# Kernel tuning notes

Measured on AMD Instinct MI355X. Metric: run time of the kernel, lower is better.

## Reference

```python
import jax, jax.numpy as jnp
import numpy as np

N_SIGMA = 1
NUM_CLASS = 1
N_INST = 16          # max instance id (ids 1..16); instances==0 is background
W_INST, W_VAR, W_SEED = 1.0, 10.0, 1.0
H, W, B = 512, 512, 8
GRID = 1024          # buffer is linspace over 1024 then cropped to H,W


def make_xym(h, w, dtype=jnp.float32):
    full = jnp.linspace(0.0, 1.0, GRID, dtype=dtype)
    xm = jnp.broadcast_to(full[:w][None, :], (h, w))   # x varies along width
    ym = jnp.broadcast_to(full[:h][:, None], (h, w))   # y varies along height
    return jnp.stack([xm, ym], axis=0)                 # [2, H, W]


def lovasz_hinge_flat(logits, labels):
    # logits: [N] float, labels: [N] float in {0,1}
    signs = 2.0 * labels - 1.0
    errors = 1.0 - logits * signs
    order = jnp.argsort(-errors)
    errors_sorted = errors[order]
    gt_sorted = labels[order]
    gts = jnp.sum(gt_sorted)
    intersection = gts - jnp.cumsum(gt_sorted)
    union = gts + jnp.cumsum(1.0 - gt_sorted)
    jaccard = 1.0 - intersection / union
    grad = jnp.concatenate([jaccard[:1], jaccard[1:] - jaccard[:-1]])
    return jnp.sum(jax.nn.relu(errors_sorted) * grad)


def _per_image(pred, instance, label, xym):
    h, w = pred.shape[1], pred.shape[2]
    spatial_emb = jnp.tanh(pred[0:2]) + xym              # [2,H,W]
    sigma = pred[2:2 + N_SIGMA]                          # [n_sigma,H,W]
    seed = jax.nn.sigmoid(pred[2 + N_SIGMA])             # [H,W] (num_class==1)

    label_mask = (label == 1)
    bg_mask = (label == 0)
    seed_loss = jnp.sum(jnp.where(bg_mask, seed ** 2, 0.0))

    ids = jnp.arange(1, N_INST + 1)
    masks = (instance[None] == ids[:, None, None]) & label_mask[None]  # [K,H,W] bool
    maskf = masks.astype(pred.dtype)
    counts = jnp.sum(maskf, axis=(1, 2))                 # [K]
    present = counts > 0
    safe = jnp.maximum(counts, 1.0)

    # to_center=True: center = mean of xym coords over each instance mask
    center = jnp.einsum('khw,chw->kc', maskf, xym) / safe[:, None]        # [K,2]
    s_mean = jnp.einsum('khw,shw->ks', maskf, sigma) / safe[:, None]      # [K,n_sigma]

    # var loss: mean over in-mask pixels of (sigma - detached mean)^2
    dev2 = (sigma[None] - jax.lax.stop_gradient(s_mean)[:, :, None, None]) ** 2  # [K,ns,H,W]
    var_terms = jnp.einsum('khw,kshw->k', maskf, dev2) / (safe * N_SIGMA)

    # dist = exp(-s * sum_c (emb_c - center_c)^2), s = exp(10 * mean sigma)
    s_exp = jnp.exp(10.0 * s_mean)[:, 0]                 # [K] (n_sigma==1 broadcasts)
    diff2 = jnp.sum((spatial_emb[None] - center[:, :, None, None]) ** 2, axis=1)  # [K,H,W]
    dist = jnp.exp(-s_exp[:, None, None] * diff2)        # [K,H,W]

    inst_losses = jax.vmap(
        lambda d, m: lovasz_hinge_flat(2.0 * d.ravel() - 1.0, m.ravel())
    )(dist, maskf)
    instance_loss = jnp.sum(jnp.where(present, inst_losses, 0.0))
    var_loss = jnp.sum(jnp.where(present, var_terms, 0.0))

    seed_loss = seed_loss + jnp.sum(
        maskf * (seed[None] - jax.lax.stop_gradient(dist)) ** 2)

    obj = jnp.maximum(jnp.sum(present.astype(pred.dtype)), 1.0)
    return (W_INST * instance_loss / obj
            + W_VAR * var_loss / obj
            + W_SEED * seed_loss / (h * w))


def setup_inputs() -> dict:
    key = jax.random.key(0)
    k1, k2, k3 = jax.random.split(key, 3)
    prediction = jax.random.normal(k1, (B, 2 + N_SIGMA + NUM_CLASS, H, W), dtype=jnp.float32)
    instances = jax.random.randint(k2, (B, H, W), 0, N_INST + 1).astype(jnp.int64)
    labels = jax.random.randint(k3, (B, H, W), 0, NUM_CLASS + 1).astype(jnp.int64)
    return {"prediction": prediction, "instances": instances, "labels": labels}


def reference(prediction, instances, labels):
    xym = make_xym(prediction.shape[2], prediction.shape[3], prediction.dtype)
    per_img = jax.vmap(_per_image, in_axes=(0, 0, 0, None))(
        prediction, instances, labels, xym)
    return jnp.mean(per_img)
```

## Files before the change

### kernel.cpp

```cpp
#include <hip/hip_runtime.h>
#include <hip/hip_fp16.h>
#include <math.h>

#define HWPX 262144
#define NIMG 8
#define ACC_STRIDE 96
#define NB 1024
#define ZMAX 8.0f
#define NSPLIT 32
#define NGRP 2
#define PREP_GRID 2048

typedef unsigned long long u64;

__device__ __forceinline__ float tanh_fast(float x) {
  float t = __expf(2.0f * x);
  return 1.0f - __fdividef(2.0f, t + 1.0f);
}
__device__ __forceinline__ float sigmoid_fast(float x) {
  return __fdividef(1.0f, 1.0f + __expf(-x));
}

template<bool PACK>
__global__ __launch_bounds__(256, 2) void k_prep(const float* __restrict__ pred,
    const int* __restrict__ inst, const int* __restrict__ lab,
    u64* __restrict__ rec, float* __restrict__ part)
{
  __shared__ float s[8][83];
  int t = threadIdx.x;
  for (int i = t; i < 8*83; i += 256) (&s[0][0])[i] = 0.0f;
  __syncthreads();
  int bid = blockIdx.x;
  int b = bid >> 8;
  int px0 = ((bid & 255) << 10) + t*4;
  const float* pb = pred + (size_t)b*4*HWPX;
  size_t ib = (size_t)b*HWPX;
  int r = t & 7;
  int w0 = px0 & 511;
  float ym = (float)(px0 >> 9) * (1.0f/1023.0f);

  float4 X  = *(const float4*)(pb + px0);
  float4 Y  = *(const float4*)(pb + HWPX + px0);
  float4 Gv = *(const float4*)(pb + 2*HWPX + px0);
  float4 Q  = *(const float4*)(pb + 3*HWPX + px0);
  int4   L  = *(const int4*)(lab + ib + px0);
  int4   I  = *(const int4*)(inst + ib + px0);

  float bg = 0.0f;
  u64 rv0 = 0, rv1 = 0, rv2 = 0, rv3 = 0;

#define PXB(RV, C, XX, YY, GG, QQ, LL, II) { \
    float xm = (float)(w0 + C) * (1.0f/1023.0f); \
    float sd = sigmoid_fast(QQ); \
    int mid = ((LL) == 1 && (unsigned)((II)-1) < 16u) ? (II) : 0; \
    if (PACK) { \
      float ex = tanh_fast(XX) + xm; \
      float ey = tanh_fast(YY) + ym; \
      RV = (u64)__half_as_ushort(__float2half(ex)) \
         | ((u64)__half_as_ushort(__float2half(ey)) << 16) \
         | ((u64)__half_as_ushort(__float2half(sd)) << 32) \
         | ((u64)mid << 48); \
    } \
    if ((LL) == 0) { bg += sd*sd; } \
    else if (mid) { int k = mid - 1; \
      atomicAdd(&s[r][k], 1.0f); \
      atomicAdd(&s[r][16+k], xm); \
      atomicAdd(&s[r][32+k], ym); \
      atomicAdd(&s[r][48+k], GG); \
      atomicAdd(&s[r][64+k], (GG)*(GG)); } }

  PXB(rv0, 0, X.x, Y.x, Gv.x, Q.x, L.x, I.x)
  PXB(rv1, 1, X.y, Y.y, Gv.y, Q.y, L.y, I.y)
  PXB(rv2, 2, X.z, Y.z, Gv.z, Q.z, L.z, I.z)
  PXB(rv3, 3, X.w, Y.w, Gv.w, Q.w, L.w, I.w)
#undef PXB

  if (PACK) {
    ulonglong2* rp = (ulonglong2*)(rec + ib + px0);
    rp[0] = make_ulonglong2(rv0, rv1);
    rp[1] = make_ulonglong2(rv2, rv3);
  }
  #pragma unroll
  for (int o = 32; o > 0; o >>= 1) bg += __shfl_down(bg, o);
  if ((t & 63) == 0) atomicAdd(&s[0][80], bg);
  __syncthreads();
  if (t < 96) {
    float v = 0.0f;
    if (t < 83) {
      #pragma unroll
      for (int rr = 0; rr < 8; ++rr) v += s[rr][t];
    }
    part[(size_t)bid*96 + t] = v;
  }
}

__global__ __launch_bounds__(1024) void k_fin(const float* __restrict__ part,
    double* __restrict__ accd, float* __restrict__ pairinfo)
{
  __shared__ float red2[10*96];
  int t = threadIdx.x, b = blockIdx.x;
  if (t < 960) {
    int e = t % 96, c = t / 96;
    int lo = c*26, hi = lo + 26; if (hi > 256) hi = 256;
    const float* pp = part + (size_t)b*256*96 + e;
    float v = 0.0f;
    for (int blk = lo; blk < hi; ++blk) v += pp[(size_t)blk*96];
    red2[c*96 + e] = v;
  }
  __syncthreads();
  if (t < 96) {
    float v = 0.0f;
    #pragma unroll
    for (int cc = 0; cc < 10; ++cc) v += red2[cc*96 + t];
    red2[t] = v;
  }
  __syncthreads();
  if (t < 16) {
    float cnt = red2[t];
    float safe = cnt > 0.0f ? cnt : 1.0f;
    float sm = red2[48+t] / safe;
    float4 pi = make_float4(red2[16+t]/safe, red2[32+t]/safe, __expf(10.0f*sm), cnt);
    ((float4*)pairinfo)[b*16 + t] = pi;
  }
  if (t == 0) {
    double vs = 0.0; float np = 0.0f;
    for (int k2 = 0; k2 < 16; ++k2) {
      float cnt = red2[k2];
      if (cnt > 0.0f) {
        np += 1.0f;
        float ssg = red2[48+k2];
        float var = (red2[64+k2] - ssg*ssg/cnt) / cnt;
        if (var < 0.0f) var = 0.0f;
        vs += (double)var;
      }
    }
    double* ab = accd + (size_t)b*ACC_STRIDE;
    ab[80] = (double)red2[80];
    ab[81] = 0.0;
    ab[82] = 0.0;
    ab[83] = vs;
    ab[84] = np > 1.0f ? (double)np : 1.0;
  }
}

__global__ __launch_bounds__(1024) void k_hist(const u64* __restrict__ rec,
    const float* __restrict__ pairinfo,
    unsigned* __restrict__ partial, double* __restrict__ accd)
{
  __shared__ unsigned hist[8*NB];
  __shared__ float redf[16];
  int t = threadIdx.x, bid = blockIdx.x;
  int b = bid & 7;
  int rr = bid >> 3;
  int g = rr & 1;
  int s = rr >> 1;
  for (int i = t; i < 8*NB; i += 1024) hist[i] = 0u;
  float cx[8], cy[8], se[8], s128[8];
  #pragma unroll
  for (int j = 0; j < 8; ++j) {
    float4 pi = ((const float4*)pairinfo)[b*16 + g*8 + j];
    cx[j] = pi.x; cy[j] = pi.y; se[j] = pi.z; s128[j] = pi.z * (float)(NB/ZMAX);
  }
  __syncthreads();
  size_t base = (size_t)b*HWPX + (size_t)s*(HWPX/NSPLIT);
  float fit = 0.0f;
  for (int it = 0; it < HWPX/NSPLIT/2048; ++it) {
    size_t px = base + it*2048 + t*2;
    ulonglong2 v2 = *((const ulonglong2*)(rec + px));
    u64 vv[2] = {v2.x, v2.y};
    #pragma unroll
    for (int c = 0; c < 2; ++c) {
      u64 v = vv[c];
      float ex = __half2float(__ushort_as_half((unsigned short)(v & 0xffffu)));
      float ey = __half2float(__ushort_as_half((unsigned short)((v >> 16) & 0xffffu)));
      float sd = __half2float(__ushort_as_half((unsigned short)((v >> 32) & 0xffffu)));
      int rel = (int)(v >> 48) - 1 - g*8;
      #pragma unroll
      for (int j = 0; j < 8; ++j) {
        float dx = ex - cx[j], dy = ey - cy[j];
        float d2 = fmaf(dx, dx, dy*dy);
        int key; unsigned add;
        if (rel == j) {
          float d = __expf(-d2 * se[j]);
          float e = fmaf(-2.0f, d, 2.0f);
          int kk = (int)(e * (float)(NB/2));
          key = kk > NB-1 ? NB-1 : kk;
          add = 0x10000u;
          float df = sd - d; fit += df*df;
        } else {
          key = (int)fminf(d2 * s128[j], (float)(NB-1));
          add = 1u;
        }
        atomicAdd(&hist[j*NB + key], add);
      }
    }
  }
  #pragma unroll
  for (int o = 32; o > 0; o >>= 1) fit += __shfl_down(fit, o);
  if ((t & 63) == 0) redf[t >> 6] = fit;
  __syncthreads();
  if (t == 0) {
    float ft = 0.0f;
    for (int i = 0; i < 16; ++i) ft += redf[i];
    atomicAdd(&accd[(size_t)b*ACC_STRIDE + 81], (double)ft);
  }
  unsigned* pp = partial + (size_t)((b*NGRP + g)*NSPLIT + s)*(8*NB);
  for (int i = t; i < 8*NB; i += 1024) pp[i] = hist[i];
}

__global__ __launch_bounds__(1024) void k_scan(const unsigned* __restrict__ partial,
    const float* __restrict__ pairinfo, double* __restrict__ accd)
{
  __shared__ unsigned sp[NB], sq[NB];
  __shared__ float red[16];
  int t = threadIdx.x, bid = blockIdx.x;
  int b = bid >> 4, k = bid & 15;
  int g = k >> 3, j8 = k & 7;
  float G = pairinfo[(b*16 + k)*4 + 3];
  if (G <= 0.0f) return;
  sq[t] = 0u;
  __syncthreads();
  unsigned p = 0, q = 0;
  const unsigned* basep = partial + (size_t)((b*NGRP + g)*NSPLIT)*(8*NB) + j8*NB + t;
  #pragma unroll 4
  for (int s2 = 0; s2 < NSPLIT; ++s2) {
    unsigned h = basep[(size_t)s2*(8*NB)];
    p += h >> 16; q += h & 0xffffu;
  }
  float zmid = (t + 0.5f) * (ZMAX/NB);
  float ev = 2.0f * __expf(-zmid);
  int eb = (int)(ev * (float)(NB/2));
  if (eb > NB-1) eb = NB-1;
  if (q) atomicAdd(&sq[eb], q);
  __syncthreads();
  unsigned qe = sq[t];
  __syncthreads();
  int j = (NB-1) - t;
  sp[j] = p; sq[j] = qe;
  __syncthreads();
  for (int off = 1; off < NB; off <<= 1) {
    unsigned vp = 0, vq = 0;
    if (j >= off) { vp = sp[j-off]; vq = sq[j-off]; }
    __syncthreads();
    sp[j] += vp; sq[j] += vq;
    __syncthreads();
  }
  float A  = (float)(sp[j] - p);
  float Bn = (float)(sq[j] - qe);
  float val = (t + 0.5f) * (2.0f/NB);
  float pf = (float)p, qf = (float)qe;
  float Jb = (A + Bn) / (G + Bn);
  float Ja = (A + Bn + pf + qf) / (G + Bn + qf);
  float contrib = val * (Ja - Jb);
  #pragma unroll
  for (int o = 32; o > 0; o >>= 1) contrib += __shfl_down(contrib, o);
  if ((t & 63) == 0) red[t >> 6] = contrib;
  __syncthreads();
  if (t == 0) {
    float tot = 0.0f;
    for (int i = 0; i < 16; ++i) tot += red[i];
    atomicAdd(&accd[(size_t)b*ACC_STRIDE + 82], (double)tot);
  }
}

__global__ __launch_bounds__(1024) void k_lov_old(const float* __restrict__ pred,
    const int* __restrict__ inst, const int* __restrict__ lab,
    const float* __restrict__ pairinfo, double* __restrict__ accd)
{
  constexpr int SHIFT = 18;
  constexpr int NBB = (0x40000000 >> SHIFT) + 1;
  extern __shared__ unsigned char smem[];
  unsigned* histP = reinterpret_cast<unsigned*>(smem);
  unsigned* histQ = histP + NBB;
  unsigned* scanP = histQ + NBB;
  unsigned* scanQ = scanP + 1024;
  float* red  = reinterpret_cast<float*>(scanQ + 1024);
  float* redf = red + 16;
  int t = threadIdx.x, bid = blockIdx.x;
  int b = bid >> 4, k = bid & 15;
  float4 pi = reinterpret_cast<const float4*>(pairinfo)[bid];
  float cx = pi.x, cy = pi.y, sexp = pi.z, G = pi.w;
  if (G <= 0.0f) return;
  for (int i = t; i < 2*NBB; i += 1024) histP[i] = 0u;
  __syncthreads();
  size_t ib = (size_t)b * HWPX;
  const float* pb = pred + (size_t)b * 4 * HWPX;
  const int target = k + 1;
  float fit = 0.0f;
  for (int j = 0; j < HWPX/1024; ++j) {
    int px = (j << 10) + t;
    int h = px >> 9, w = px & 511;
    float ex = tanhf(pb[px]) + w*(1.0f/1023.0f);
    float ey = tanhf(pb[HWPX+px]) + h*(1.0f/1023.0f);
    float sd = 1.0f/(1.0f + __expf(-pb[3*HWPX+px]));
    int lv = lab[ib+px], iv = inst[ib+px];
    float dx = ex - cx, dy = ey - cy;
    float d = __expf(-sexp * (dx*dx + dy*dy));
    bool m = (lv == 1) && (iv == target);
    float e = m ? fmaf(-2.0f, d, 2.0f) : 2.0f * d;
    unsigned key = __float_as_uint(e) >> SHIFT;
    atomicAdd(m ? &histP[key] : &histQ[key], 1u);
    if (m) { float df = sd - d; fit += df*df; }
  }
  #pragma unroll
  for (int o = 32; o > 0; o >>= 1) fit += __shfl_down(fit, o);
  if ((t & 63) == 0) redf[t >> 6] = fit;
  __syncthreads();
  constexpr int CB = NBB / 1024;
  int start = (NBB - 1) - t * CB;
  int nk = (t == 1023) ? (CB + 1) : CB;
  unsigned lp = 0, lq = 0;
  for (int i = 0; i < nk; ++i) { lp += histP[start-i]; lq += histQ[start-i]; }
  scanP[t] = lp; scanQ[t] = lq;
  __syncthreads();
  for (int off = 1; off < 1024; off <<= 1) {
    unsigned vp = 0, vq = 0;
    if (t >= off) { vp = scanP[t-off]; vq = scanQ[t-off]; }
    __syncthreads();
    scanP[t] += vp; scanQ[t] += vq;
    __syncthreads();
  }
  float A  = (float)(scanP[t] - lp);
  float Bn = (float)(scanQ[t] - lq);
  float contrib = 0.0f;
  for (int i = 0; i < nk; ++i) {
    int kk = start - i;
    unsigned p = histP[kk], q = histQ[kk];
    if (p | q) {
      float lo = __uint_as_float((unsigned)kk << SHIFT);
      float hi = __uint_as_float((unsigned)(kk+1) << SHIFT);
      float valv = 0.5f*(lo+hi);
      if (valv > 2.0f) valv = 2.0f;
      float pq = (float)(p + q), qf = (float)q;
      float Jb = (A + Bn) / (G + Bn);
      float Ja = (A + Bn + pq) / (G + Bn + qf);
      contrib += valv * (Ja - Jb);
      A += (float)p; Bn += qf;
    }
  }
  #pragma unroll
  for (int o = 32; o > 0; o >>= 1) contrib += __shfl_down(contrib, o);
  if ((t & 63) == 0) red[t >> 6] = contrib;
  __syncthreads();
  if (t == 0) {
    float tot = 0.0f, ft = 0.0f;
    for (int i = 0; i < 16; ++i) { tot += red[i]; ft += redf[i]; }
    atomicAdd(&accd[(size_t)b*ACC_STRIDE + 82], (double)tot);
    atomicAdd(&accd[(size_t)b*ACC_STRIDE + 81], (double)ft);
  }
}

__global__ void k_final(const double* __restrict__ accd, float* __restrict__ out)
{
  int t = threadIdx.x;
  double lb = 0.0;
  if (t < NIMG) {
    const double* ab = accd + (size_t)t*ACC_STRIDE;
    lb = (ab[82] + 10.0*ab[83]) / ab[84] + (ab[80] + ab[81]) * (1.0/(double)HWPX);
  }
  #pragma unroll
  for (int o = 4; o > 0; o >>= 1) lb += __shfl_down(lb, o);
  if (t == 0) out[0] = (float)(lb * 0.125);
}

extern "C" void kernel_launch(void* const* d_in, const int* in_sizes, int n_in,
                              void* d_out, int out_size, void* d_ws, size_t ws_size,
                              hipStream_t stream)
{
  const float* pred = (const float*)d_in[0];
  const int*   inst = (const int*)d_in[1];
  const int*   lab  = (const int*)d_in[2];
  float* out = (float*)d_out;

  size_t recB   = (size_t)NIMG * HWPX * sizeof(u64);
  size_t partB  = (size_t)NIMG * NGRP * NSPLIT * 8 * NB * 4;
  size_t pstatB = (size_t)PREP_GRID * 96 * sizeof(float);
  size_t accB   = (size_t)NIMG * ACC_STRIDE * sizeof(double);
  size_t pairB  = 128 * 4 * sizeof(float);
  bool full = ws_size >= recB + partB + pstatB + accB + pairB;

  char* ws = (char*)d_ws;
  if (full) {
    u64*      rec   = (u64*)ws;
    unsigned* part  = (unsigned*)(ws + recB);
    float*    pstat = (float*)(ws + recB + partB);
    double*   accd  = (double*)(ws + recB + partB + pstatB);
    float*    pairinfo = (float*)(ws + recB + partB + pstatB + accB);
    k_prep<true><<<PREP_GRID,256,0,stream>>>(pred, inst, lab, rec, pstat);
    k_fin<<<NIMG,1024,0,stream>>>(pstat, accd, pairinfo);
    k_hist<<<NIMG*NGRP*NSPLIT,1024,0,stream>>>(rec, pairinfo, part, accd);
    k_scan<<<128,1024,0,stream>>>(part, pairinfo, accd);
    k_final<<<1,64,0,stream>>>(accd, out);
  } else {
    float*    pstat = (float*)ws;
    double*   accd  = (double*)(ws + pstatB);
    float*    pairinfo = (float*)(ws + pstatB + accB);
    k_prep<false><<<PREP_GRID,256,0,stream>>>(pred, inst, lab, nullptr, pstat);
    k_fin<<<NIMG,1024,0,stream>>>(pstat, accd, pairinfo);
    size_t lds18 = ((size_t)2*4097 + 2048)*4 + 128;
    k_lov_old<<<128,1024,lds18,stream>>>(pred, inst, lab, pairinfo, accd);
    k_final<<<1,64,0,stream>>>(accd, out);
  }
}
```

Baseline: 73.55 us.

## Recompute embeddings in histogram kernel instead of storing packed fp16 records

Drops the intermediate packed fp16 record buffer. The histogram kernel now reads the raw prediction, instance and label arrays and recomputes tanh, sigmoid and embeddings itself, covering all 16 instances per block rather than splitting them into two groups of 8. Histogram resolution is halved to 512 bins and the split count doubled, so each block handles 4 pixels per thread, and the scan kernel runs with 512 threads. This removes the 16MB record write and read, at the cost of more transcendental math per pixel-instance pair and coarser loss quantisation.

```diff
diff --git a/kernel.cpp b/kernel.cpp
--- a/kernel.cpp
+++ b/kernel.cpp
@@ -1,14 +1,12 @@
 #include <hip/hip_runtime.h>
-#include <hip/hip_fp16.h>
 #include <math.h>
 
 #define HWPX 262144
 #define NIMG 8
 #define ACC_STRIDE 96
-#define NB 1024
+#define NB 512
 #define ZMAX 8.0f
-#define NSPLIT 32
-#define NGRP 2
+#define NSPLIT 64
 #define PREP_GRID 2048
 
 typedef unsigned long long u64;
@@ -21,10 +19,9 @@
   return __fdividef(1.0f, 1.0f + __expf(-x));
 }
 
-template<bool PACK>
-__global__ __launch_bounds__(256, 2) void k_prep(const float* __restrict__ pred,
+__global__ __launch_bounds__(256) void k_stats(const float* __restrict__ pred,
     const int* __restrict__ inst, const int* __restrict__ lab,
-    u64* __restrict__ rec, float* __restrict__ part)
+    float* __restrict__ part)
 {
   __shared__ float s[8][83];
   int t = threadIdx.x;
@@ -39,47 +36,28 @@
   int w0 = px0 & 511;
   float ym = (float)(px0 >> 9) * (1.0f/1023.0f);
 
-  float4 X  = *(const float4*)(pb + px0);
-  float4 Y  = *(const float4*)(pb + HWPX + px0);
   float4 Gv = *(const float4*)(pb + 2*HWPX + px0);
   float4 Q  = *(const float4*)(pb + 3*HWPX + px0);
   int4   L  = *(const int4*)(lab + ib + px0);
   int4   I  = *(const int4*)(inst + ib + px0);
 
   float bg = 0.0f;
-  u64 rv0 = 0, rv1 = 0, rv2 = 0, rv3 = 0;
-
-#define PXB(RV, C, XX, YY, GG, QQ, LL, II) { \
+#define PXS(C, GG, QQ, LL, II) { \
     float xm = (float)(w0 + C) * (1.0f/1023.0f); \
-    float sd = sigmoid_fast(QQ); \
     int mid = ((LL) == 1 && (unsigned)((II)-1) < 16u) ? (II) : 0; \
-    if (PACK) { \
-      float ex = tanh_fast(XX) + xm; \
-      float ey = tanh_fast(YY) + ym; \
-      RV = (u64)__half_as_ushort(__float2half(ex)) \
-         | ((u64)__half_as_ushort(__float2half(ey)) << 16) \
-         | ((u64)__half_as_ushort(__float2half(sd)) << 32) \
-         | ((u64)mid << 48); \
-    } \
-    if ((LL) == 0) { bg += sd*sd; } \
+    if ((LL) == 0) { float sd = sigmoid_fast(QQ); bg += sd*sd; } \
     else if (mid) { int k = mid - 1; \
       atomicAdd(&s[r][k], 1.0f); \
       atomicAdd(&s[r][16+k], xm); \
       atomicAdd(&s[r][32+k], ym); \
       atomicAdd(&s[r][48+k], GG); \
       atomicAdd(&s[r][64+k], (GG)*(GG)); } }
-
-  PXB(rv0, 0, X.x, Y.x, Gv.x, Q.x, L.x, I.x)
-  PXB(rv1, 1, X.y, Y.y, Gv.y, Q.y, L.y, I.y)
-  PXB(rv2, 2, X.z, Y.z, Gv.z, Q.z, L.z, I.z)
-  PXB(rv3, 3, X.w, Y.w, Gv.w, Q.w, L.w, I.w)
-#undef PXB
-
-  if (PACK) {
-    ulonglong2* rp = (ulonglong2*)(rec + ib + px0);
-    rp[0] = make_ulonglong2(rv0, rv1);
-    rp[1] = make_ulonglong2(rv2, rv3);
-  }
+  PXS(0, Gv.x, Q.x, L.x, I.x)
+  PXS(1, Gv.y, Q.y, L.y, I.y)
+  PXS(2, Gv.z, Q.z, L.z, I.z)
+  PXS(3, Gv.w, Q.w, L.w, I.w)
+#undef PXS
+
   #pragma unroll
   for (int o = 32; o > 0; o >>= 1) bg += __shfl_down(bg, o);
   if ((t & 63) == 0) atomicAdd(&s[0][80], bg);
@@ -143,58 +121,60 @@
   }
 }
 
-__global__ __launch_bounds__(1024) void k_hist(const u64* __restrict__ rec,
+__global__ __launch_bounds__(1024, 4) void k_hist(const float* __restrict__ pred,
+    const int* __restrict__ inst, const int* __restrict__ lab,
     const float* __restrict__ pairinfo,
     unsigned* __restrict__ partial, double* __restrict__ accd)
 {
-  __shared__ unsigned hist[8*NB];
+  __shared__ unsigned hist[16*NB];
   __shared__ float redf[16];
   int t = threadIdx.x, bid = blockIdx.x;
   int b = bid & 7;
-  int rr = bid >> 3;
-  int g = rr & 1;
-  int s = rr >> 1;
-  for (int i = t; i < 8*NB; i += 1024) hist[i] = 0u;
-  float cx[8], cy[8], se[8], s128[8];
-  #pragma unroll
-  for (int j = 0; j < 8; ++j) {
-    float4 pi = ((const float4*)pairinfo)[b*16 + g*8 + j];
-    cx[j] = pi.x; cy[j] = pi.y; se[j] = pi.z; s128[j] = pi.z * (float)(NB/ZMAX);
-  }
-  __syncthreads();
-  size_t base = (size_t)b*HWPX + (size_t)s*(HWPX/NSPLIT);
+  int s = bid >> 3;
+  for (int i = t; i < 16*NB; i += 1024) hist[i] = 0u;
+  float cx[16], cy[16], s128[16];
+  #pragma unroll
+  for (int j = 0; j < 16; ++j) {
+    float4 pi = ((const float4*)pairinfo)[b*16 + j];
+    cx[j] = pi.x; cy[j] = pi.y; s128[j] = pi.z * (float)(NB/ZMAX);
+  }
+  __syncthreads();
+  int px0 = s*(HWPX/NSPLIT) + t*4;
+  const float* pb = pred + (size_t)b*4*HWPX;
+  size_t ib = (size_t)b*HWPX;
+  float4 X = *(const float4*)(pb + px0);
+  float4 Y = *(const float4*)(pb + HWPX + px0);
+  float4 Q = *(const float4*)(pb + 3*HWPX + px0);
+  int4   L = *(const int4*)(lab + ib + px0);
+  int4   I = *(const int4*)(inst + ib + px0);
+  int w0 = px0 & 511;
+  float ym = (float)(px0 >> 9) * (1.0f/1023.0f);
   float fit = 0.0f;
-  for (int it = 0; it < HWPX/NSPLIT/2048; ++it) {
-    size_t px = base + it*2048 + t*2;
-    ulonglong2 v2 = *((const ulonglong2*)(rec + px));
-    u64 vv[2] = {v2.x, v2.y};
-    #pragma unroll
-    for (int c = 0; c < 2; ++c) {
-      u64 v = vv[c];
-      float ex = __half2float(__ushort_as_half((unsigned short)(v & 0xffffu)));
-      float ey = __half2float(__ushort_as_half((unsigned short)((v >> 16) & 0xffffu)));
-      float sd = __half2float(__ushort_as_half((unsigned short)((v >> 32) & 0xffffu)));
-      int rel = (int)(v >> 48) - 1 - g*8;
-      #pragma unroll
-      for (int j = 0; j < 8; ++j) {
-        float dx = ex - cx[j], dy = ey - cy[j];
-        float d2 = fmaf(dx, dx, dy*dy);
-        int key; unsigned add;
-        if (rel == j) {
-          float d = __expf(-d2 * se[j]);
-          float e = fmaf(-2.0f, d, 2.0f);
-          int kk = (int)(e * (float)(NB/2));
-          key = kk > NB-1 ? NB-1 : kk;
-          add = 0x10000u;
-          float df = sd - d; fit += df*df;
-        } else {
-          key = (int)fminf(d2 * s128[j], (float)(NB-1));
-          add = 1u;
-        }
-        atomicAdd(&hist[j*NB + key], add);
-      }
-    }
-  }
+
+#define PXH(C, XX, YY, QQ, LL, II) { \
+    float xm = (float)(w0 + C) * (1.0f/1023.0f); \
+    float exf = tanh_fast(XX) + xm; \
+    float eyf = tanh_fast(YY) + ym; \
+    float sd = sigmoid_fast(QQ); \
+    int rel = ((LL) == 1 && (unsigned)((II)-1) < 16u) ? ((II)-1) : -1; \
+    _Pragma("unroll") \
+    for (int j = 0; j < 16; ++j) { \
+      float dx = exf - cx[j], dy = eyf - cy[j]; \
+      float z = fmaf(dx, dx, dy*dy) * s128[j]; \
+      float d = __expf(-z * (ZMAX/(float)NB)); \
+      bool m = (j == rel); \
+      float e = fmaf(-2.0f, d, 2.0f); \
+      int kp = (int)(e * (float)(NB/2)); kp = kp > NB-1 ? NB-1 : kp; \
+      int kn = (int)fminf(z, (float)(NB-1)); \
+      atomicAdd(&hist[j*NB + (m ? kp : kn)], m ? 0x10000u : 1u); \
+      if (m) { float df = sd - d; fit += df*df; } \
+    } }
+  PXH(0, X.x, Y.x, Q.x, L.x, I.x)
+  PXH(1, X.y, Y.y, Q.y, L.y, I.y)
+  PXH(2, X.z, Y.z, Q.z, L.z, I.z)
+  PXH(3, X.w, Y.w, Q.w, L.w, I.w)
+#undef PXH
+
   #pragma unroll
   for (int o = 32; o > 0; o >>= 1) fit += __shfl_down(fit, o);
   if ((t & 63) == 0) redf[t >> 6] = fit;
@@ -204,27 +184,26 @@
     for (int i = 0; i < 16; ++i) ft += redf[i];
     atomicAdd(&accd[(size_t)b*ACC_STRIDE + 81], (double)ft);
   }
-  unsigned* pp = partial + (size_t)((b*NGRP + g)*NSPLIT + s)*(8*NB);
-  for (int i = t; i < 8*NB; i += 1024) pp[i] = hist[i];
-}
-
-__global__ __launch_bounds__(1024) void k_scan(const unsigned* __restrict__ partial,
+  unsigned* pp = partial + (size_t)(b*NSPLIT + s)*(16*NB);
+  for (int i = t; i < 16*NB; i += 1024) pp[i] = hist[i];
+}
+
+__global__ __launch_bounds__(512) void k_scan(const unsigned* __restrict__ partial,
     const float* __restrict__ pairinfo, double* __restrict__ accd)
 {
   __shared__ unsigned sp[NB], sq[NB];
-  __shared__ float red[16];
+  __shared__ float red[8];
   int t = threadIdx.x, bid = blockIdx.x;
   int b = bid >> 4, k = bid & 15;
-  int g = k >> 3, j8 = k & 7;
   float G = pairinfo[(b*16 + k)*4 + 3];
   if (G <= 0.0f) return;
   sq[t] = 0u;
   __syncthreads();
   unsigned p = 0, q = 0;
-  const unsigned* basep = partial + (size_t)((b*NGRP + g)*NSPLIT)*(8*NB) + j8*NB + t;
+  const unsigned* basep = partial + (size_t)(b*NSPLIT)*(16*NB) + k*NB + t;
   #pragma unroll 4
   for (int s2 = 0; s2 < NSPLIT; ++s2) {
-    unsigned h = basep[(size_t)s2*(8*NB)];
+    unsigned h = basep[(size_t)s2*(16*NB)];
     p += h >> 16; q += h & 0xffffu;
   }
   float zmid = (t + 0.5f) * (ZMAX/NB);
@@ -258,7 +237,7 @@
   __syncthreads();
   if (t == 0) {
     float tot = 0.0f;
-    for (int i = 0; i < 16; ++i) tot += red[i];
+    for (int i = 0; i < 8; ++i) tot += red[i];
     atomicAdd(&accd[(size_t)b*ACC_STRIDE + 82], (double)tot);
   }
 }
@@ -372,30 +351,28 @@
   const int*   lab  = (const int*)d_in[2];
   float* out = (float*)d_out;
 
-  size_t recB   = (size_t)NIMG * HWPX * sizeof(u64);
-  size_t partB  = (size_t)NIMG * NGRP * NSPLIT * 8 * NB * 4;
+  size_t partB  = (size_t)NIMG * NSPLIT * 16 * NB * 4;
   size_t pstatB = (size_t)PREP_GRID * 96 * sizeof(float);
   size_t accB   = (size_t)NIMG * ACC_STRIDE * sizeof(double);
   size_t pairB  = 128 * 4 * sizeof(float);
-  bool full = ws_size >= recB + partB + pstatB + accB + pairB;
+  bool full = ws_size >= partB + pstatB + accB + pairB;
 
   char* ws = (char*)d_ws;
   if (full) {
-    u64*      rec   = (u64*)ws;
-    unsigned* part  = (unsigned*)(ws + recB);
-    float*    pstat = (float*)(ws + recB + partB);
-    double*   accd  = (double*)(ws + recB + partB + pstatB);
-    float*    pairinfo = (float*)(ws + recB + partB + pstatB + accB);
-    k_prep<true><<<PREP_GRID,256,0,stream>>>(pred, inst, lab, rec, pstat);
+    unsigned* part  = (unsigned*)ws;
+    float*    pstat = (float*)(ws + partB);
+    double*   accd  = (double*)(ws + partB + pstatB);
+    float*    pairinfo = (float*)(ws + partB + pstatB + accB);
+    k_stats<<<PREP_GRID,256,0,stream>>>(pred, inst, lab, pstat);
     k_fin<<<NIMG,1024,0,stream>>>(pstat, accd, pairinfo);
-    k_hist<<<NIMG*NGRP*NSPLIT,1024,0,stream>>>(rec, pairinfo, part, accd);
-    k_scan<<<128,1024,0,stream>>>(part, pairinfo, accd);
+    k_hist<<<NIMG*NSPLIT,1024,0,stream>>>(pred, inst, lab, pairinfo, part, accd);
+    k_scan<<<128,512,0,stream>>>(part, pairinfo, accd);
     k_final<<<1,64,0,stream>>>(accd, out);
   } else {
     float*    pstat = (float*)ws;
     double*   accd  = (double*)(ws + pstatB);
     float*    pairinfo = (float*)(ws + pstatB + accB);
-    k_prep<false><<<PREP_GRID,256,0,stream>>>(pred, inst, lab, nullptr, pstat);
+    k_stats<<<PREP_GRID,256,0,stream>>>(pred, inst, lab, pstat);
     k_fin<<<NIMG,1024,0,stream>>>(pstat, accd, pairinfo);
     size_t lds18 = ((size_t)2*4097 + 2048)*4 + 128;
     k_lov_old<<<128,1024,lds18,stream>>>(pred, inst, lab, pairinfo, accd);
```

After: 81.75 us. +11.2%, slower.

## Re-partition prep and histogram grids to cut partial buffers and reduction work

Applied to the files above, without the earlier changes.

k_prep now runs 256 blocks of 1024 threads, each thread handling 8 pixels with scalar coalesced loads. This cuts the per-block statistics partials from 2048 to 256, so k_fin becomes a small 128-thread single-pass reduction. k_hist halves NSPLIT, which halves the number of 32KB per-block histograms written to global memory and later read by k_scan. The cost is fewer blocks, about one per CU, which gives less latency hiding. The vector float4/ulonglong2 loads are also replaced by scalar loads.

```diff
diff --git a/kernel.cpp b/kernel.cpp
--- a/kernel.cpp
+++ b/kernel.cpp
@@ -7,9 +7,9 @@
 #define ACC_STRIDE 96
 #define NB 1024
 #define ZMAX 8.0f
-#define NSPLIT 32
+#define NSPLIT 16
 #define NGRP 2
-#define PREP_GRID 2048
+#define PREP_BLOCKS 256
 
 typedef unsigned long long u64;
 
@@ -22,63 +22,52 @@
 }
 
 template<bool PACK>
-__global__ __launch_bounds__(256, 2) void k_prep(const float* __restrict__ pred,
+__global__ __launch_bounds__(1024) void k_prep(const float* __restrict__ pred,
     const int* __restrict__ inst, const int* __restrict__ lab,
     u64* __restrict__ rec, float* __restrict__ part)
 {
   __shared__ float s[8][83];
   int t = threadIdx.x;
-  for (int i = t; i < 8*83; i += 256) (&s[0][0])[i] = 0.0f;
+  for (int i = t; i < 8*83; i += 1024) (&s[0][0])[i] = 0.0f;
   __syncthreads();
   int bid = blockIdx.x;
-  int b = bid >> 8;
-  int px0 = ((bid & 255) << 10) + t*4;
+  int b = bid >> 5;
+  int chunk = bid & 31;
   const float* pb = pred + (size_t)b*4*HWPX;
   size_t ib = (size_t)b*HWPX;
   int r = t & 7;
-  int w0 = px0 & 511;
-  float ym = (float)(px0 >> 9) * (1.0f/1023.0f);
-
-  float4 X  = *(const float4*)(pb + px0);
-  float4 Y  = *(const float4*)(pb + HWPX + px0);
-  float4 Gv = *(const float4*)(pb + 2*HWPX + px0);
-  float4 Q  = *(const float4*)(pb + 3*HWPX + px0);
-  int4   L  = *(const int4*)(lab + ib + px0);
-  int4   I  = *(const int4*)(inst + ib + px0);
-
   float bg = 0.0f;
-  u64 rv0 = 0, rv1 = 0, rv2 = 0, rv3 = 0;
-
-#define PXB(RV, C, XX, YY, GG, QQ, LL, II) { \
-    float xm = (float)(w0 + C) * (1.0f/1023.0f); \
-    float sd = sigmoid_fast(QQ); \
-    int mid = ((LL) == 1 && (unsigned)((II)-1) < 16u) ? (II) : 0; \
-    if (PACK) { \
-      float ex = tanh_fast(XX) + xm; \
-      float ey = tanh_fast(YY) + ym; \
-      RV = (u64)__half_as_ushort(__float2half(ex)) \
-         | ((u64)__half_as_ushort(__float2half(ey)) << 16) \
-         | ((u64)__half_as_ushort(__float2half(sd)) << 32) \
-         | ((u64)mid << 48); \
-    } \
-    if ((LL) == 0) { bg += sd*sd; } \
-    else if (mid) { int k = mid - 1; \
-      atomicAdd(&s[r][k], 1.0f); \
-      atomicAdd(&s[r][16+k], xm); \
-      atomicAdd(&s[r][32+k], ym); \
-      atomicAdd(&s[r][48+k], GG); \
-      atomicAdd(&s[r][64+k], (GG)*(GG)); } }
-
-  PXB(rv0, 0, X.x, Y.x, Gv.x, Q.x, L.x, I.x)
-  PXB(rv1, 1, X.y, Y.y, Gv.y, Q.y, L.y, I.y)
-  PXB(rv2, 2, X.z, Y.z, Gv.z, Q.z, L.z, I.z)
-  PXB(rv3, 3, X.w, Y.w, Gv.w, Q.w, L.w, I.w)
-#undef PXB
-
-  if (PACK) {
-    ulonglong2* rp = (ulonglong2*)(rec + ib + px0);
-    rp[0] = make_ulonglong2(rv0, rv1);
-    rp[1] = make_ulonglong2(rv2, rv3);
+  #pragma unroll
+  for (int j = 0; j < 8; ++j) {
+    int px = (chunk << 13) + (j << 10) + t;
+    float X = pb[px];
+    float Y = pb[HWPX + px];
+    float Gv = pb[2*HWPX + px];
+    float Q = pb[3*HWPX + px];
+    int L = lab[ib + px];
+    int I = inst[ib + px];
+    int w = px & 511, h = px >> 9;
+    float xm = (float)w * (1.0f/1023.0f), ym = (float)h * (1.0f/1023.0f);
+    float sd = sigmoid_fast(Q);
+    int mid = (L == 1 && (unsigned)(I-1) < 16u) ? I : 0;
+    if (PACK) {
+      float ex = tanh_fast(X) + xm;
+      float ey = tanh_fast(Y) + ym;
+      rec[ib + px] = (u64)__half_as_ushort(__float2half(ex))
+                   | ((u64)__half_as_ushort(__float2half(ey)) << 16)
+                   | ((u64)__half_as_ushort(__float2half(sd)) << 32)
+                   | ((u64)mid << 48);
+    }
+    if (L == 0) {
+      bg += sd*sd;
+    } else if (mid) {
+      int k = mid - 1;
+      atomicAdd(&s[r][k], 1.0f);
+      atomicAdd(&s[r][16+k], xm);
+      atomicAdd(&s[r][32+k], ym);
+      atomicAdd(&s[r][48+k], Gv);
+      atomicAdd(&s[r][64+k], Gv*Gv);
+    }
   }
   #pragma unroll
   for (int o = 32; o > 0; o >>= 1) bg += __shfl_down(bg, o);
@@ -86,7 +75,7 @@
   __syncthreads();
   if (t < 96) {
     float v = 0.0f;
-    if (t < 83) {
+    if (t < 81) {
       #pragma unroll
       for (int rr = 0; rr < 8; ++rr) v += s[rr][t];
     }
@@ -94,48 +83,40 @@
   }
 }
 
-__global__ __launch_bounds__(1024) void k_fin(const float* __restrict__ part,
+__global__ __launch_bounds__(128) void k_fin(const float* __restrict__ part,
     double* __restrict__ accd, float* __restrict__ pairinfo)
 {
-  __shared__ float red2[10*96];
+  __shared__ float red[96];
   int t = threadIdx.x, b = blockIdx.x;
-  if (t < 960) {
-    int e = t % 96, c = t / 96;
-    int lo = c*26, hi = lo + 26; if (hi > 256) hi = 256;
-    const float* pp = part + (size_t)b*256*96 + e;
-    float v = 0.0f;
-    for (int blk = lo; blk < hi; ++blk) v += pp[(size_t)blk*96];
-    red2[c*96 + e] = v;
-  }
-  __syncthreads();
   if (t < 96) {
     float v = 0.0f;
-    #pragma unroll
-    for (int cc = 0; cc < 10; ++cc) v += red2[cc*96 + t];
-    red2[t] = v;
+    const float* pp = part + (size_t)b*32*96 + t;
+    #pragma unroll 8
+    for (int blk = 0; blk < 32; ++blk) v += pp[(size_t)blk*96];
+    red[t] = v;
   }
   __syncthreads();
   if (t < 16) {
-    float cnt = red2[t];
+    float cnt = red[t];
     float safe = cnt > 0.0f ? cnt : 1.0f;
-    float sm = red2[48+t] / safe;
-    float4 pi = make_float4(red2[16+t]/safe, red2[32+t]/safe, __expf(10.0f*sm), cnt);
+    float sm = red[48+t] / safe;
+    float4 pi = make_float4(red[16+t]/safe, red[32+t]/safe, __expf(10.0f*sm), cnt);
     ((float4*)pairinfo)[b*16 + t] = pi;
   }
   if (t == 0) {
     double vs = 0.0; float np = 0.0f;
     for (int k2 = 0; k2 < 16; ++k2) {
-      float cnt = red2[k2];
+      float cnt = red[k2];
       if (cnt > 0.0f) {
         np += 1.0f;
-        float ssg = red2[48+k2];
-        float var = (red2[64+k2] - ssg*ssg/cnt) / cnt;
+        float ssg = red[48+k2];
+        float var = (red[64+k2] - ssg*ssg/cnt) / cnt;
         if (var < 0.0f) var = 0.0f;
         vs += (double)var;
       }
     }
     double* ab = accd + (size_t)b*ACC_STRIDE;
-    ab[80] = (double)red2[80];
+    ab[80] = (double)red[80];
     ab[81] = 0.0;
     ab[82] = 0.0;
     ab[83] = vs;
@@ -159,40 +140,36 @@
   #pragma unroll
   for (int j = 0; j < 8; ++j) {
     float4 pi = ((const float4*)pairinfo)[b*16 + g*8 + j];
-    cx[j] = pi.x; cy[j] = pi.y; se[j] = pi.z; s128[j] = pi.z * (float)(NB/ZMAX);
+    cx[j] = pi.x; cy[j] = pi.y; se[j] = pi.z; s128[j] = pi.z * ((float)NB/ZMAX);
   }
   __syncthreads();
   size_t base = (size_t)b*HWPX + (size_t)s*(HWPX/NSPLIT);
   float fit = 0.0f;
-  for (int it = 0; it < HWPX/NSPLIT/2048; ++it) {
-    size_t px = base + it*2048 + t*2;
-    ulonglong2 v2 = *((const ulonglong2*)(rec + px));
-    u64 vv[2] = {v2.x, v2.y};
+  #pragma unroll 2
+  for (int it = 0; it < HWPX/NSPLIT/1024; ++it) {
+    size_t px = base + it*1024 + t;
+    u64 v = rec[px];
+    float ex = __half2float(__ushort_as_half((unsigned short)(v & 0xffffu)));
+    float ey = __half2float(__ushort_as_half((unsigned short)((v >> 16) & 0xffffu)));
+    float sd = __half2float(__ushort_as_half((unsigned short)((v >> 32) & 0xffffu)));
+    int rel = (int)(v >> 48) - 1 - g*8;
     #pragma unroll
-    for (int c = 0; c < 2; ++c) {
-      u64 v = vv[c];
-      float ex = __half2float(__ushort_as_half((unsigned short)(v & 0xffffu)));
-      float ey = __half2float(__ushort_as_half((unsigned short)((v >> 16) & 0xffffu)));
-      float sd = __half2float(__ushort_as_half((unsigned short)((v >> 32) & 0xffffu)));
-      int rel = (int)(v >> 48) - 1 - g*8;
-      #pragma unroll
-      for (int j = 0; j < 8; ++j) {
-        float dx = ex - cx[j], dy = ey - cy[j];
-        float d2 = fmaf(dx, dx, dy*dy);
-        int key; unsigned add;
-        if (rel == j) {
-          float d = __expf(-d2 * se[j]);
-          float e = fmaf(-2.0f, d, 2.0f);
-          int kk = (int)(e * (float)(NB/2));
-          key = kk > NB-1 ? NB-1 : kk;
-          add = 0x10000u;
-          float df = sd - d; fit += df*df;
-        } else {
-          key = (int)fminf(d2 * s128[j], (float)(NB-1));
-          add = 1u;
-        }
-        atomicAdd(&hist[j*NB + key], add);
+    for (int j = 0; j < 8; ++j) {
+      float dx = ex - cx[j], dy = ey - cy[j];
+      float d2 = fmaf(dx, dx, dy*dy);
+      int key; unsigned add;
+      if (rel == j) {
+        float d = __expf(-d2 * se[j]);
+        float e = fmaf(-2.0f, d, 2.0f);
+        int kk = (int)(e * (float)(NB/2));
+        key = kk > NB-1 ? NB-1 : kk;
+        add = 0x10000u;
+        float df = sd - d; fit += df*df;
+      } else {
+        key = (int)fminf(d2 * s128[j], (float)(NB-1));
+        add = 1u;
       }
+      atomicAdd(&hist[j*NB + key], add);
     }
   }
   #pragma unroll
@@ -374,7 +351,7 @@
 
   size_t recB   = (size_t)NIMG * HWPX * sizeof(u64);
   size_t partB  = (size_t)NIMG * NGRP * NSPLIT * 8 * NB * 4;
-  size_t pstatB = (size_t)PREP_GRID * 96 * sizeof(float);
+  size_t pstatB = (size_t)PREP_BLOCKS * 96 * sizeof(float);
   size_t accB   = (size_t)NIMG * ACC_STRIDE * sizeof(double);
   size_t pairB  = 128 * 4 * sizeof(float);
   bool full = ws_size >= recB + partB + pstatB + accB + pairB;
@@ -386,8 +363,8 @@
     float*    pstat = (float*)(ws + recB + partB);
     double*   accd  = (double*)(ws + recB + partB + pstatB);
     float*    pairinfo = (float*)(ws + recB + partB + pstatB + accB);
-    k_prep<true><<<PREP_GRID,256,0,stream>>>(pred, inst, lab, rec, pstat);
-    k_fin<<<NIMG,1024,0,stream>>>(pstat, accd, pairinfo);
+    k_prep<true><<<PREP_BLOCKS,1024,0,stream>>>(pred, inst, lab, rec, pstat);
+    k_fin<<<NIMG,128,0,stream>>>(pstat, accd, pairinfo);
     k_hist<<<NIMG*NGRP*NSPLIT,1024,0,stream>>>(rec, pairinfo, part, accd);
     k_scan<<<128,1024,0,stream>>>(part, pairinfo, accd);
     k_final<<<1,64,0,stream>>>(accd, out);
@@ -395,8 +372,8 @@
     float*    pstat = (float*)ws;
     double*   accd  = (double*)(ws + pstatB);
     float*    pairinfo = (float*)(ws + pstatB + accB);
-    k_prep<false><<<PREP_GRID,256,0,stream>>>(pred, inst, lab, nullptr, pstat);
-    k_fin<<<NIMG,1024,0,stream>>>(pstat, accd, pairinfo);
+    k_prep<false><<<PREP_BLOCKS,1024,0,stream>>>(pred, inst, lab, nullptr, pstat);
+    k_fin<<<NIMG,128,0,stream>>>(pstat, accd, pairinfo);
     size_t lds18 = ((size_t)2*4097 + 2048)*4 + 128;
     k_lov_old<<<128,1024,lds18,stream>>>(pred, inst, lab, pairinfo, accd);
     k_final<<<1,64,0,stream>>>(accd, out);
```

After: 65.70 us (median of 2 runs). 10.7% less time.
